# Optimization experiments

Measured on AMD Instinct MI355X. Metric: run time of the kernel, lower is better.

Reference implementation:

```python
import jax, jax.numpy as jnp
import numpy as np

V, L_MAX, D_MODEL, N_LAYER, N_STATE, EXPAND = 49408, 512, 768, 4, 16, 2
D_INNER = EXPAND * D_MODEL            # 1536
DT_RANK = -(-D_MODEL // 16)           # 48 ('auto' = ceil(d_model/16))
D_CONV = 4
B, T = 4, 256
EPS = 1e-5


def setup_inputs() -> dict:
    key = jax.random.key(0)
    ks = jax.random.split(key, 10)
    s = 0.02
    inp = {
        "input_ids": jax.random.randint(ks[0], (B, T), 0, V),
        "emb": jax.random.normal(ks[1], (V, D_MODEL), jnp.float32) * s,
        "pos_emb": jax.random.normal(ks[2], (1, L_MAX, D_MODEL), jnp.float32) * s,
        "in_proj_w": jax.random.normal(ks[3], (N_LAYER, 2 * D_INNER, D_MODEL), jnp.float32) * s,
        "conv_w": jax.random.normal(ks[4], (N_LAYER, D_INNER, D_CONV), jnp.float32) * s,
        "conv_b": jnp.zeros((N_LAYER, D_INNER), jnp.float32),
        "x_proj_w": jax.random.normal(ks[5], (N_LAYER, DT_RANK + 2 * N_STATE, D_INNER), jnp.float32) * s,
        "dt_proj_w": jax.random.normal(ks[6], (N_LAYER, D_INNER, DT_RANK), jnp.float32) * s,
        "dt_proj_b": jnp.full((N_LAYER, D_INNER), -4.6, jnp.float32),  # softplus(-4.6)~0.01, inside [dt_min,dt_max]
        # S4D-real init: A_log[l,d,n] = log(n+1)
        "A_log": jnp.tile(jnp.log(jnp.arange(1, N_STATE + 1, dtype=jnp.float32)), (N_LAYER, D_INNER, 1)),
        "D_skip": jnp.ones((N_LAYER, D_INNER), jnp.float32),
        "out_proj_w": jax.random.normal(ks[7], (N_LAYER, D_MODEL, D_INNER), jnp.float32) * s,
        "norm_w": jnp.ones((D_MODEL,), jnp.float32),
    }
    return inp


def _causal_dwconv(x, w, b):
    # x: (B, C, T), w: (C, K) depthwise, b: (C,) ; causal pad K-1 on the left
    out = jax.lax.conv_general_dilated(
        x, w[:, None, :], window_strides=(1,), padding=[(D_CONV - 1, 0)],
        feature_group_count=x.shape[1], dimension_numbers=("NCH", "OIH", "NCH"))
    return out + b[None, :, None]


def _selective_scan(deltaA, dBx, Cm):
    # deltaA, dBx: (B, T, D, N); Cm: (B, T, N) -> y: (B, T, D)
    def step(h, t_in):
        dA, dbx, c = t_in
        h = dA * h + dbx                          # (B, D, N)
        y = jnp.einsum("bdn,bn->bd", h, c)
        return h, y
    h0 = jnp.zeros(deltaA.shape[:1] + deltaA.shape[2:], deltaA.dtype)
    _, ys = jax.lax.scan(step, h0, (deltaA.swapaxes(0, 1), dBx.swapaxes(0, 1), Cm.swapaxes(0, 1)))
    return ys.swapaxes(0, 1)


def _mamba_block(x, ipw, cw, cb, xpw, dpw, dpb, A_log, Dp, opw):
    # x: (B, T, d_model)
    xz = jnp.einsum("btd,ed->bte", x, ipw)        # (B, T, 2*D_INNER)
    xi, z = jnp.split(xz, 2, axis=-1)
    xi = jax.nn.silu(_causal_dwconv(xi.swapaxes(1, 2), cw, cb)).swapaxes(1, 2)  # (B, T, D_INNER)
    x_dbl = jnp.einsum("btd,ed->bte", xi, xpw)    # (B, T, DT_RANK + 2N)
    dt, Bm, Cm = jnp.split(x_dbl, [DT_RANK, DT_RANK + N_STATE], axis=-1)
    dt = jax.nn.softplus(jnp.einsum("btr,dr->btd", dt, dpw) + dpb)              # (B, T, D_INNER)
    A = -jnp.exp(A_log)                            # (D_INNER, N)
    deltaA = jnp.exp(dt[..., None] * A)            # (B, T, D_INNER, N)
    dBx = dt[..., None] * Bm[:, :, None, :] * xi[..., None]                     # (B, T, D_INNER, N)
    y = _selective_scan(deltaA, dBx, Cm) + Dp * xi
    y = y * jax.nn.silu(z)
    return jnp.einsum("btd,ed->bte", y, opw)       # (B, T, d_model)


def reference(input_ids, emb, pos_emb, in_proj_w, conv_w, conv_b, x_proj_w,
              dt_proj_w, dt_proj_b, A_log, D_skip, out_proj_w, norm_w):
    Tlen = input_ids.shape[1]
    x = emb[input_ids] + pos_emb[:, :Tlen, :]
    for l in range(N_LAYER):
        x = x + _mamba_block(x, in_proj_w[l], conv_w[l], conv_b[l], x_proj_w[l],
                             dt_proj_w[l], dt_proj_b[l], A_log[l], D_skip[l], out_proj_w[l])
    # RMSNormGated with no gate -> plain RMSNorm
    x = x * jax.lax.rsqrt(jnp.mean(x * x, axis=-1, keepdims=True) + EPS) * norm_w
    return x
```

## Files before the change

### kernel.cpp

```cpp
#include <hip/hip_runtime.h>
#include <math.h>

#define TLEN 256
#define BATCH 4
#define DMODEL 768
#define DINNER 1536
#define NSTATE 16
#define DTRANK 48
#define NLAYER 4
#define NTOK 1024

#define S_IP 2359296
#define S_OP 1179648
#define S_XP2 196608
#define S_DT 98304
#define WL (S_IP + S_OP + S_XP2 + S_DT)

typedef __bf16 bf16x8 __attribute__((ext_vector_type(8)));
typedef float f32x4 __attribute__((ext_vector_type(4)));

__device__ inline unsigned short f2b(float f) {
    union { float f; unsigned u; } v;
    v.f = f;
    unsigned r = (v.u + 0x7fffu + ((v.u >> 16) & 1u)) >> 16;
    return (unsigned short)r;
}

__device__ inline void gload16(const void* g, void* l) {
    __builtin_amdgcn_global_load_lds(
        (const __attribute__((address_space(1))) void*)g,
        (__attribute__((address_space(3))) void*)l, 16, 0, 0);
}

__device__ inline float red16(float p) {
    p += __int_as_float(__builtin_amdgcn_update_dpp(0, __float_as_int(p), 0xB1, 0xf, 0xf, true));
    p += __int_as_float(__builtin_amdgcn_update_dpp(0, __float_as_int(p), 0x4E, 0xf, 0xf, true));
    p += __int_as_float(__builtin_amdgcn_update_dpp(0, __float_as_int(p), 0x124, 0xf, 0xf, true));
    p += __int_as_float(__builtin_amdgcn_update_dpp(0, __float_as_int(p), 0x128, 0xf, 0xf, true));
    return p;
}

__global__ __launch_bounds__(256) void embed_k(const int* __restrict__ ids,
                                               const float* __restrict__ emb,
                                               const float* __restrict__ pos,
                                               float* __restrict__ x,
                                               unsigned short* __restrict__ xb) {
    int idx = blockIdx.x * 256 + threadIdx.x;
    int d = idx % DMODEL;
    int bt = idx / DMODEL;
    int t = bt % TLEN;
    float v = emb[(size_t)ids[bt] * DMODEL + d] + pos[t * DMODEL + d];
    x[idx] = v;
    xb[idx] = f2b(v);
}

__global__ __launch_bounds__(256) void wconv_k(const float* __restrict__ ipw,
                                               const float* __restrict__ opw,
                                               const float* __restrict__ xpw,
                                               const float* __restrict__ dpw,
                                               unsigned short* __restrict__ w_all) {
    int l = blockIdx.y;
    int i4 = (blockIdx.x * 256 + threadIdx.x) * 4;
    unsigned short* wl = w_all + (size_t)l * WL;
    if (i4 < S_IP) {
        float4 v = *(const float4*)(ipw + (size_t)l * S_IP + i4);
        ushort4 o; o.x = f2b(v.x); o.y = f2b(v.y); o.z = f2b(v.z); o.w = f2b(v.w);
        *(ushort4*)(wl + i4) = o;
    } else if (i4 < S_IP + S_OP) {
        int i = i4 - S_IP;
        float4 v = *(const float4*)(opw + (size_t)l * S_OP + i);
        ushort4 o; o.x = f2b(v.x); o.y = f2b(v.y); o.z = f2b(v.z); o.w = f2b(v.w);
        *(ushort4*)(wl + S_IP + i) = o;
    } else if (i4 < S_IP + S_OP + S_XP2) {
        int i = i4 - S_IP - S_OP;
        int r = i / 1536, k = i % 1536;
        ushort4 o = {0, 0, 0, 0};
        if (r < 80) {
            float4 v = *(const float4*)(xpw + (size_t)l * (80 * 1536) + (size_t)r * 1536 + k);
            o.x = f2b(v.x); o.y = f2b(v.y); o.z = f2b(v.z); o.w = f2b(v.w);
        }
        *(ushort4*)(wl + S_IP + S_OP + i) = o;
    } else {
        int i = i4 - S_IP - S_OP - S_XP2;
        int r = i >> 6, k = i & 63;
        ushort4 o = {0, 0, 0, 0};
        if (k < DTRANK) {
            float4 v = *(const float4*)(dpw + (size_t)l * (DINNER * DTRANK) + (size_t)r * DTRANK + k);
            o.x = f2b(v.x); o.y = f2b(v.y); o.z = f2b(v.z); o.w = f2b(v.w);
        }
        *(ushort4*)(wl + S_IP + S_OP + S_XP2 + i) = o;
    }
}

template <int BM, int MODE>
__global__ __launch_bounds__(256) void mgemm_k(const unsigned short* __restrict__ A, int lda,
                                               const unsigned short* __restrict__ B, int ldb,
                                               int K,
                                               const float* __restrict__ bias,
                                               float* __restrict__ o0,
                                               unsigned short* __restrict__ o1) {
    constexpr int MI = BM / 32;
    __shared__ __align__(16) unsigned short Ab[2][BM * 64];
    __shared__ __align__(16) unsigned short Bb[2][64 * 64];
    __shared__ float Tt[(MODE == 1) ? 64 * 64 : 1];

    int tid = threadIdx.x;
    int lane = tid & 63;
    int wave = tid >> 6;
    int wm = (wave >> 1) * (BM / 2);
    int wn = (wave & 1) * 32;
    int bm = blockIdx.x * BM;
    int bn = blockIdx.y * 64;
    int fr = lane & 15;
    int fq = lane >> 4;
    int fk = fq * 8;
    int srow = lane >> 3;
    int scol = (lane & 7) * 8;

    f32x4 acc[MI][2] = {};

    auto stage = [&](int s, int k0) {
#pragma unroll
        for (int c = 0; c < BM / 32; ++c) {
            int r = wave * (BM / 4) + c * 8;
            gload16(A + (size_t)(bm + r + srow) * lda + k0 + scol, &Ab[s][r * 64]);
        }
#pragma unroll
        for (int c = 0; c < 2; ++c) {
            int r = wave * 16 + c * 8;
            gload16(B + (size_t)(bn + r + srow) * ldb + k0 + scol, &Bb[s][r * 64]);
        }
    };

    int nk = K >> 6;
    stage(0, 0);
    asm volatile("s_waitcnt vmcnt(0)" ::: "memory");
    __builtin_amdgcn_s_barrier();

    for (int t = 0; t < nk; ++t) {
        int cur = t & 1;
        if (t + 1 < nk) stage(cur ^ 1, (t + 1) * 64);
#pragma unroll
        for (int ks = 0; ks < 2; ++ks) {
            int kk = ks * 32 + fk;
            bf16x8 af[MI], bfr[2];
#pragma unroll
            for (int i = 0; i < MI; ++i)
                af[i] = *(const bf16x8*)&Ab[cur][(wm + i * 16 + fr) * 64 + kk];
#pragma unroll
            for (int j = 0; j < 2; ++j)
                bfr[j] = *(const bf16x8*)&Bb[cur][(wn + j * 16 + fr) * 64 + kk];
#pragma unroll
            for (int i = 0; i < MI; ++i)
#pragma unroll
                for (int j = 0; j < 2; ++j)
                    acc[i][j] = __builtin_amdgcn_mfma_f32_16x16x32_bf16(
                        af[i], bfr[j], acc[i][j], 0, 0, 0);
        }
        asm volatile("s_waitcnt vmcnt(0)" ::: "memory");
        __builtin_amdgcn_s_barrier();
    }

#pragma unroll
    for (int i = 0; i < MI; ++i) {
#pragma unroll
        for (int j = 0; j < 2; ++j) {
            int lc = wn + j * 16 + fr;
#pragma unroll
            for (int q = 0; q < 4; ++q) {
                int lr = wm + i * 16 + fq * 4 + q;
                float v = acc[i][j][q];
                if (MODE == 0) {
                    o0[(size_t)(bm + lr) * NTOK + bn + lc] = v;
                } else if (MODE == 1) {
                    int f = bm + lr;
                    if (f < 80) o0[(size_t)f * NTOK + bn + lc] = v;
                    Tt[lc * 64 + lr] = v;
                } else if (MODE == 2) {
                    float s = v + bias[bm + lr];
                    s = (s > 0.f) ? s + log1pf(__expf(-s)) : log1pf(__expf(s));
                    o0[(size_t)(bm + lr) * NTOK + bn + lc] = s;
                } else {
                    size_t idx = (size_t)(bm + lr) * DMODEL + bn + lc;
                    float nv = o0[idx] + v;
                    o0[idx] = nv;
                    o1[idx] = f2b(nv);
                }
            }
        }
    }
    if (MODE == 1) {
        __syncthreads();
        if (bm == 0) {
            int tok = tid >> 2;
            int fb = (tid & 3) * 16;
#pragma unroll
            for (int vv = 0; vv < 4; ++vv) {
                int f0 = fb + vv * 4;
                ushort4 o;
                o.x = f2b(Tt[tok * 64 + f0 + 0]);
                o.y = f2b(Tt[tok * 64 + f0 + 1]);
                o.z = f2b(Tt[tok * 64 + f0 + 2]);
                o.w = f2b(Tt[tok * 64 + f0 + 3]);
                *(ushort4*)(o1 + (size_t)(bn + tok) * 64 + f0) = o;
            }
        }
    }
}

__global__ __launch_bounds__(256) void conv_k(const float* __restrict__ xzT,
                                              const float* __restrict__ cw,
                                              const float* __restrict__ cb,
                                              unsigned short* __restrict__ xib) {
    __shared__ unsigned short tile[4][256];
    int tid = threadIdx.x;
    int ch = tid >> 6;
    int d = blockIdx.x * 4 + ch;
    int b = blockIdx.y;
    int t0 = (tid & 63) * 4;
    const float* src = xzT + (size_t)d * NTOK + b * TLEN + t0;
    float4 cur = *(const float4*)src;
    float4 prev = {0.f, 0.f, 0.f, 0.f};
    if (t0 > 0) prev = *(const float4*)(src - 4);
    float w0 = cw[d * 4 + 0], w1 = cw[d * 4 + 1], w2 = cw[d * 4 + 2], w3 = cw[d * 4 + 3];
    float bb = cb[d];
    float xw[8] = {prev.x, prev.y, prev.z, prev.w, cur.x, cur.y, cur.z, cur.w};
#pragma unroll
    for (int u = 0; u < 4; ++u) {
        float s = bb + w0 * xw[u + 1] + w1 * xw[u + 2] + w2 * xw[u + 3] + w3 * xw[u + 4];
        float v = s / (1.f + __expf(-s));
        tile[ch][t0 + u] = f2b(v);
    }
    __syncthreads();
    int t = tid;
    ushort4 o;
    o.x = tile[0][t]; o.y = tile[1][t]; o.z = tile[2][t]; o.w = tile[3][t];
    *(ushort4*)(xib + (size_t)(b * TLEN + t) * DINNER + blockIdx.x * 4) = o;
}

__global__ __launch_bounds__(512) void scan_k(const float* __restrict__ dtT,
                                              const float* __restrict__ xzT,
                                              const float* __restrict__ xdblT,
                                              const float* __restrict__ cw,
                                              const float* __restrict__ cb,
                                              const float* __restrict__ Alog,
                                              const float* __restrict__ Dsk,
                                              unsigned short* __restrict__ ybb) {
    __shared__ float yl[4][260];
    __shared__ float cum[4][260];
    __shared__ float hL[8][4][16];
    __shared__ float Pb[8][4][16];
    __shared__ float Hin[8][4][16];

    int tid = threadIdx.x;
    int c = tid >> 6;
    int lane = tid & 63;
    int ch = lane >> 4;
    int n = lane & 15;
    int d = blockIdx.x * 4 + ch;
    int b = blockIdx.y;
    int tl0 = c * 32;

    float a = -__expf(Alog[(size_t)d * NSTATE + n]);
    float Dv = Dsk[d];
    float w0 = cw[d * 4 + 0], w1 = cw[d * 4 + 1], w2 = cw[d * 4 + 2], w3 = cw[d * 4 + 3];
    float cbv = cb[d];
    const float* dtp = dtT + (size_t)d * NTOK + b * TLEN + tl0;
    const float* xzp = xzT + (size_t)d * NTOK + b * TLEN + tl0;
    const float* Bp = xdblT + (size_t)(DTRANK + n) * NTOK + b * TLEN + tl0;
    const float* Cp = xdblT + (size_t)(DTRANK + NSTATE + n) * NTOK + b * TLEN + tl0;

    float hm3 = 0.f, hm2 = 0.f, hm1 = 0.f;
    if (tl0 > 0) {
        float4 pv = *(const float4*)(xzp - 4);
        hm3 = pv.y; hm2 = pv.z; hm1 = pv.w;
    }

    float h = 0.f, cd = 0.f;
    for (int t8 = 0; t8 < 32; t8 += 8) {
        float4 d0 = *(const float4*)(dtp + t8), d1 = *(const float4*)(dtp + t8 + 4);
        float4 x0 = *(const float4*)(xzp + t8), x1 = *(const float4*)(xzp + t8 + 4);
        float4 B0 = *(const float4*)(Bp + t8), B1 = *(const float4*)(Bp + t8 + 4);
        float4 C0 = *(const float4*)(Cp + t8), C1 = *(const float4*)(Cp + t8 + 4);
        float dts[8] = {d0.x, d0.y, d0.z, d0.w, d1.x, d1.y, d1.z, d1.w};
        float xw[11] = {hm3, hm2, hm1, x0.x, x0.y, x0.z, x0.w, x1.x, x1.y, x1.z, x1.w};
        float Bs[8] = {B0.x, B0.y, B0.z, B0.w, B1.x, B1.y, B1.z, B1.w};
        float Cs[8] = {C0.x, C0.y, C0.z, C0.w, C1.x, C1.y, C1.z, C1.w};
#pragma unroll
        for (int u = 0; u < 8; ++u) {
            float s = cbv + w0 * xw[u] + w1 * xw[u + 1] + w2 * xw[u + 2] + w3 * xw[u + 3];
            float xi = s / (1.f + __expf(-s));
            float dtv = dts[u];
            cd += dtv;
            float dA = __expf(dtv * a);
            h = dA * h + (dtv * xi) * Bs[u];
            float p = red16(h * Cs[u]);
            if (n == 0) {
                yl[ch][tl0 + t8 + u] = p + Dv * xi;
                cum[ch][tl0 + t8 + u] = cd;
            }
        }
        hm3 = xw[8]; hm2 = xw[9]; hm1 = xw[10];
    }
    hL[c][ch][n] = h;
    Pb[c][ch][n] = __expf(a * cd);
    __syncthreads();
    if (c == 0) {
        float H = 0.f;
        Hin[0][ch][n] = 0.f;
#pragma unroll
        for (int cc = 1; cc < 8; ++cc) {
            H = Pb[cc - 1][ch][n] * H + hL[cc - 1][ch][n];
            Hin[cc][ch][n] = H;
        }
    }
    __syncthreads();
    float Hv = Hin[c][ch][n];
    const float* zp = xzT + (size_t)(DINNER + d) * NTOK + b * TLEN + tl0;
    for (int t8 = 0; t8 < 32; t8 += 8) {
        float4 C0 = *(const float4*)(Cp + t8), C1 = *(const float4*)(Cp + t8 + 4);
        float4 z0 = *(const float4*)(zp + t8), z1 = *(const float4*)(zp + t8 + 4);
        float Cs[8] = {C0.x, C0.y, C0.z, C0.w, C1.x, C1.y, C1.z, C1.w};
        float zs[8] = {z0.x, z0.y, z0.z, z0.w, z1.x, z1.y, z1.z, z1.w};
#pragma unroll
        for (int u = 0; u < 8; ++u) {
            float cdt = cum[ch][tl0 + t8 + u];
            float corr = red16(Cs[u] * __expf(a * cdt) * Hv);
            if (n == 0) {
                float y = yl[ch][tl0 + t8 + u] + corr;
                float zz = zs[u];
                y *= zz / (1.f + __expf(-zz));
                yl[ch][tl0 + t8 + u] = y;
            }
        }
    }
    __syncthreads();
    if (tid < 256) {
        int t = tid;
        ushort4 o;
        o.x = f2b(yl[0][t]);
        o.y = f2b(yl[1][t]);
        o.z = f2b(yl[2][t]);
        o.w = f2b(yl[3][t]);
        *(ushort4*)(ybb + (size_t)(b * TLEN + t) * DINNER + blockIdx.x * 4) = o;
    }
}

__global__ __launch_bounds__(256) void rmsnorm_k(const float* __restrict__ x,
                                                 const float* __restrict__ nw,
                                                 float* __restrict__ out) {
    int row = blockIdx.x;
    const float* xr = x + (size_t)row * DMODEL;
    int tid = threadIdx.x;
    float s = 0.f;
    for (int d = tid; d < DMODEL; d += 256) {
        float v = xr[d];
        s += v * v;
    }
#pragma unroll
    for (int off = 32; off >= 1; off >>= 1) s += __shfl_down(s, off);
    __shared__ float red[4];
    __shared__ float scale;
    int wid = tid >> 6, lane = tid & 63;
    if (lane == 0) red[wid] = s;
    __syncthreads();
    if (tid == 0) {
        float tot = red[0] + red[1] + red[2] + red[3];
        scale = rsqrtf(tot / (float)DMODEL + 1e-5f);
    }
    __syncthreads();
    float sc = scale;
    for (int d = tid; d < DMODEL; d += 256)
        out[(size_t)row * DMODEL + d] = xr[d] * sc * nw[d];
}

extern "C" void kernel_launch(void* const* d_in, const int* in_sizes, int n_in,
                              void* d_out, int out_size, void* d_ws, size_t ws_size,
                              hipStream_t stream) {
    const int* ids = (const int*)d_in[0];
    const float* emb = (const float*)d_in[1];
    const float* pos = (const float*)d_in[2];
    const float* ipw = (const float*)d_in[3];
    const float* cw = (const float*)d_in[4];
    const float* cb = (const float*)d_in[5];
    const float* xpw = (const float*)d_in[6];
    const float* dpw = (const float*)d_in[7];
    const float* dpb = (const float*)d_in[8];
    const float* Alog = (const float*)d_in[9];
    const float* Dsk = (const float*)d_in[10];
    const float* opw = (const float*)d_in[11];
    const float* nw = (const float*)d_in[12];

    float* x = (float*)d_ws;
    float* xzT = x + 786432;
    float* xdblT = xzT + 3145728;
    float* dtT = xdblT + 81920;
    unsigned short* xb = (unsigned short*)(dtT + 1572864);
    unsigned short* xib = xb + 786432;
    unsigned short* ybb = xib + 1572864;
    unsigned short* xdblb = ybb + 1572864;
    unsigned short* w_all = xdblb + 65536;

    wconv_k<<<dim3(WL / 1024, NLAYER), 256, 0, stream>>>(ipw, opw, xpw, dpw, w_all);
    embed_k<<<NTOK * DMODEL / 256, 256, 0, stream>>>(ids, emb, pos, x, xb);

    for (int l = 0; l < NLAYER; ++l) {
        const unsigned short* w_ip = w_all + (size_t)l * WL;
        const unsigned short* w_op = w_ip + S_IP;
        const unsigned short* w_xp = w_op + S_OP;
        const unsigned short* w_dt = w_xp + S_XP2;
        const float* cw_l = cw + (size_t)l * DINNER * 4;
        const float* cb_l = cb + (size_t)l * DINNER;
        const float* dpb_l = dpb + (size_t)l * DINNER;
        const float* Alog_l = Alog + (size_t)l * DINNER * NSTATE;
        const float* Dsk_l = Dsk + (size_t)l * DINNER;

        mgemm_k<64, 0><<<dim3(3072 / 64, NTOK / 64), 256, 0, stream>>>(
            w_ip, DMODEL, xb, DMODEL, DMODEL, nullptr, xzT, nullptr);
        conv_k<<<dim3(DINNER / 4, BATCH), 256, 0, stream>>>(xzT, cw_l, cb_l, xib);
        mgemm_k<64, 1><<<dim3(2, NTOK / 64), 256, 0, stream>>>(
            w_xp, DINNER, xib, DINNER, DINNER, nullptr, xdblT, xdblb);
        mgemm_k<64, 2><<<dim3(DINNER / 64, NTOK / 64), 256, 0, stream>>>(
            w_dt, 64, xdblb, 64, 64, dpb_l, dtT, nullptr);
        scan_k<<<dim3(DINNER / 4, BATCH), 512, 0, stream>>>(
            dtT, xzT, xdblT, cw_l, cb_l, Alog_l, Dsk_l, ybb);
        mgemm_k<64, 3><<<dim3(NTOK / 64, DMODEL / 64), 256, 0, stream>>>(
            ybb, DINNER, w_op, DINNER, DINNER, nullptr, x, xb);
    }

    rmsnorm_k<<<NTOK, 256, 0, stream>>>(x, nw, (float*)d_out);
}
```

Before: 527.2 us.

## Fuse conv into x_proj GEMM, fold dt_proj, store activations in bf16

Depthwise conv + SiLU is computed on the fly while staging the x_proj GEMM's B operand. The dt projection with softplus is then run inside the same kernel using the x_dbl tile kept in shared memory. The xz and dt intermediates are stored as bf16 instead of fp32 to halve their memory traffic, and the weight conversion and embedding kernels are merged into one launch. This removes separate conv and dt GEMM launches and their intermediate round trips. The cost is that the fused kernel runs only 16 blocks serially over all dt tiles, and bf16 storage loses some precision.

```diff
diff --git a/kernel.cpp b/kernel.cpp
--- a/kernel.cpp
+++ b/kernel.cpp
@@ -15,6 +15,9 @@
 #define S_XP2 196608
 #define S_DT 98304
 #define WL (S_IP + S_OP + S_XP2 + S_DT)
+#define NB_W (WL / 1024)
+#define NB_WALL (NB_W * NLAYER)
+#define NB_E (NTOK * DMODEL / 256)
 
 typedef __bf16 bf16x8 __attribute__((ext_vector_type(8)));
 typedef float f32x4 __attribute__((ext_vector_type(4)));
@@ -24,6 +27,11 @@
     v.f = f;
     unsigned r = (v.u + 0x7fffu + ((v.u >> 16) & 1u)) >> 16;
     return (unsigned short)r;
+}
+__device__ inline float b2f(unsigned short u) {
+    union { unsigned u; float f; } v;
+    v.u = ((unsigned)u) << 16;
+    return v.f;
 }
 
 __device__ inline void gload16(const void* g, void* l) {
@@ -40,27 +48,30 @@
     return p;
 }
 
-__global__ __launch_bounds__(256) void embed_k(const int* __restrict__ ids,
-                                               const float* __restrict__ emb,
-                                               const float* __restrict__ pos,
-                                               float* __restrict__ x,
-                                               unsigned short* __restrict__ xb) {
-    int idx = blockIdx.x * 256 + threadIdx.x;
-    int d = idx % DMODEL;
-    int bt = idx / DMODEL;
-    int t = bt % TLEN;
-    float v = emb[(size_t)ids[bt] * DMODEL + d] + pos[t * DMODEL + d];
-    x[idx] = v;
-    xb[idx] = f2b(v);
-}
-
-__global__ __launch_bounds__(256) void wconv_k(const float* __restrict__ ipw,
-                                               const float* __restrict__ opw,
-                                               const float* __restrict__ xpw,
-                                               const float* __restrict__ dpw,
-                                               unsigned short* __restrict__ w_all) {
-    int l = blockIdx.y;
-    int i4 = (blockIdx.x * 256 + threadIdx.x) * 4;
+__global__ __launch_bounds__(256) void prep_k(const float* __restrict__ ipw,
+                                              const float* __restrict__ opw,
+                                              const float* __restrict__ xpw,
+                                              const float* __restrict__ dpw,
+                                              const int* __restrict__ ids,
+                                              const float* __restrict__ emb,
+                                              const float* __restrict__ pos,
+                                              unsigned short* __restrict__ w_all,
+                                              float* __restrict__ x,
+                                              unsigned short* __restrict__ xb) {
+    int bid = blockIdx.x;
+    int tid = threadIdx.x;
+    if (bid >= NB_WALL) {
+        int idx = (bid - NB_WALL) * 256 + tid;
+        int d = idx % DMODEL;
+        int bt = idx / DMODEL;
+        int t = bt % TLEN;
+        float v = emb[(size_t)ids[bt] * DMODEL + d] + pos[t * DMODEL + d];
+        x[idx] = v;
+        xb[idx] = f2b(v);
+        return;
+    }
+    int l = bid / NB_W;
+    int i4 = ((bid % NB_W) * 256 + tid) * 4;
     unsigned short* wl = w_all + (size_t)l * WL;
     if (i4 < S_IP) {
         float4 v = *(const float4*)(ipw + (size_t)l * S_IP + i4);
@@ -92,24 +103,21 @@
     }
 }
 
-template <int BM, int MODE>
+template <int MODE>
 __global__ __launch_bounds__(256) void mgemm_k(const unsigned short* __restrict__ A, int lda,
                                                const unsigned short* __restrict__ B, int ldb,
                                                int K,
-                                               const float* __restrict__ bias,
                                                float* __restrict__ o0,
                                                unsigned short* __restrict__ o1) {
-    constexpr int MI = BM / 32;
-    __shared__ __align__(16) unsigned short Ab[2][BM * 64];
+    __shared__ __align__(16) unsigned short Ab[2][64 * 64];
     __shared__ __align__(16) unsigned short Bb[2][64 * 64];
-    __shared__ float Tt[(MODE == 1) ? 64 * 64 : 1];
 
     int tid = threadIdx.x;
     int lane = tid & 63;
     int wave = tid >> 6;
-    int wm = (wave >> 1) * (BM / 2);
+    int wm = (wave >> 1) * 32;
     int wn = (wave & 1) * 32;
-    int bm = blockIdx.x * BM;
+    int bm = blockIdx.x * 64;
     int bn = blockIdx.y * 64;
     int fr = lane & 15;
     int fq = lane >> 4;
@@ -117,17 +125,13 @@
     int srow = lane >> 3;
     int scol = (lane & 7) * 8;
 
-    f32x4 acc[MI][2] = {};
+    f32x4 acc[2][2] = {};
 
     auto stage = [&](int s, int k0) {
-#pragma unroll
-        for (int c = 0; c < BM / 32; ++c) {
-            int r = wave * (BM / 4) + c * 8;
-            gload16(A + (size_t)(bm + r + srow) * lda + k0 + scol, &Ab[s][r * 64]);
-        }
 #pragma unroll
         for (int c = 0; c < 2; ++c) {
             int r = wave * 16 + c * 8;
+            gload16(A + (size_t)(bm + r + srow) * lda + k0 + scol, &Ab[s][r * 64]);
             gload16(B + (size_t)(bn + r + srow) * ldb + k0 + scol, &Bb[s][r * 64]);
         }
     };
@@ -143,15 +147,15 @@
 #pragma unroll
         for (int ks = 0; ks < 2; ++ks) {
             int kk = ks * 32 + fk;
-            bf16x8 af[MI], bfr[2];
-#pragma unroll
-            for (int i = 0; i < MI; ++i)
+            bf16x8 af[2], bfr[2];
+#pragma unroll
+            for (int i = 0; i < 2; ++i)
                 af[i] = *(const bf16x8*)&Ab[cur][(wm + i * 16 + fr) * 64 + kk];
 #pragma unroll
             for (int j = 0; j < 2; ++j)
                 bfr[j] = *(const bf16x8*)&Bb[cur][(wn + j * 16 + fr) * 64 + kk];
 #pragma unroll
-            for (int i = 0; i < MI; ++i)
+            for (int i = 0; i < 2; ++i)
 #pragma unroll
                 for (int j = 0; j < 2; ++j)
                     acc[i][j] = __builtin_amdgcn_mfma_f32_16x16x32_bf16(
@@ -162,7 +166,7 @@
     }
 
 #pragma unroll
-    for (int i = 0; i < MI; ++i) {
+    for (int i = 0; i < 2; ++i) {
 #pragma unroll
         for (int j = 0; j < 2; ++j) {
             int lc = wn + j * 16 + fr;
@@ -171,15 +175,7 @@
                 int lr = wm + i * 16 + fq * 4 + q;
                 float v = acc[i][j][q];
                 if (MODE == 0) {
-                    o0[(size_t)(bm + lr) * NTOK + bn + lc] = v;
-                } else if (MODE == 1) {
-                    int f = bm + lr;
-                    if (f < 80) o0[(size_t)f * NTOK + bn + lc] = v;
-                    Tt[lc * 64 + lr] = v;
-                } else if (MODE == 2) {
-                    float s = v + bias[bm + lr];
-                    s = (s > 0.f) ? s + log1pf(__expf(-s)) : log1pf(__expf(s));
-                    o0[(size_t)(bm + lr) * NTOK + bn + lc] = s;
+                    o1[(size_t)(bm + lr) * NTOK + bn + lc] = f2b(v);
                 } else {
                     size_t idx = (size_t)(bm + lr) * DMODEL + bn + lc;
                     float nv = o0[idx] + v;
@@ -189,57 +185,179 @@
             }
         }
     }
-    if (MODE == 1) {
+}
+
+__global__ __launch_bounds__(256) void xproj_k(const unsigned short* __restrict__ xzT,
+                                               const unsigned short* __restrict__ w_xp,
+                                               const unsigned short* __restrict__ w_dt,
+                                               const float* __restrict__ dpb,
+                                               const float* __restrict__ cw,
+                                               const float* __restrict__ cb,
+                                               float* __restrict__ xdblT,
+                                               unsigned short* __restrict__ dtT) {
+    __shared__ __align__(16) unsigned short Ab[2][128 * 64];
+    __shared__ __align__(16) unsigned short Bb[2][64 * 64];
+    __shared__ __align__(16) unsigned short Tt[64 * 64];
+    __shared__ float dpb_s[DINNER];
+
+    int tid = threadIdx.x;
+    int lane = tid & 63;
+    int wave = tid >> 6;
+    int bn = blockIdx.x;
+    int tok0 = bn * 64;
+    int wm = (wave >> 1) * 64;
+    int wn = (wave & 1) * 32;
+    int fr = lane & 15;
+    int fq = lane >> 4;
+    int fk = fq * 8;
+    int srow = lane >> 3;
+    int scol = (lane & 7) * 8;
+
+    int cd_ = tid & 63;
+    int cg = tid >> 6;
+    bool atStart = ((bn & 3) == 0) && (cg == 0);
+
+    ushort4 bl[5];
+    float4 cw4;
+    float cbv;
+
+    auto stageA = [&](int s, int k0) {
+#pragma unroll
+        for (int c = 0; c < 4; ++c) {
+            int r = wave * 32 + c * 8;
+            gload16(w_xp + (size_t)(r + srow) * DINNER + k0 + scol, &Ab[s][r * 64]);
+        }
+    };
+    auto loadB = [&](int k0) {
+        int d = k0 + cd_;
+        const unsigned short* row = xzT + (size_t)d * NTOK + tok0 + cg * 16;
+        ushort4 z4 = {0, 0, 0, 0};
+        bl[0] = atStart ? z4 : *(const ushort4*)(row - 4);
+#pragma unroll
+        for (int c = 0; c < 4; ++c) bl[c + 1] = *(const ushort4*)(row + c * 4);
+        cw4 = *(const float4*)(cw + d * 4);
+        cbv = cb[d];
+    };
+    auto writeB = [&](int s) {
+        float xw[20];
+#pragma unroll
+        for (int c = 0; c < 5; ++c) {
+            xw[c * 4 + 0] = b2f(bl[c].x); xw[c * 4 + 1] = b2f(bl[c].y);
+            xw[c * 4 + 2] = b2f(bl[c].z); xw[c * 4 + 3] = b2f(bl[c].w);
+        }
+#pragma unroll
+        for (int u = 0; u < 16; ++u) {
+            float sv = cbv + cw4.x * xw[u + 1] + cw4.y * xw[u + 2] +
+                       cw4.z * xw[u + 3] + cw4.w * xw[u + 4];
+            float v = sv / (1.f + __expf(-sv));
+            Bb[s][(cg * 16 + u) * 64 + cd_] = f2b(v);
+        }
+    };
+
+    f32x4 acc[4][2] = {};
+    const int nk = DINNER / 64;
+
+    loadB(0);
+    stageA(0, 0);
+    writeB(0);
+    __syncthreads();
+
+    for (int t = 0; t < nk; ++t) {
+        int cur = t & 1;
+        if (t + 1 < nk) {
+            loadB((t + 1) * 64);
+            stageA(cur ^ 1, (t + 1) * 64);
+        }
+#pragma unroll
+        for (int ks = 0; ks < 2; ++ks) {
+            int kk = ks * 32 + fk;
+            bf16x8 af[4], bfr[2];
+#pragma unroll
+            for (int i = 0; i < 4; ++i)
+                af[i] = *(const bf16x8*)&Ab[cur][(wm + i * 16 + fr) * 64 + kk];
+#pragma unroll
+            for (int j = 0; j < 2; ++j)
+                bfr[j] = *(const bf16x8*)&Bb[cur][(wn + j * 16 + fr) * 64 + kk];
+#pragma unroll
+            for (int i = 0; i < 4; ++i)
+#pragma unroll
+                for (int j = 0; j < 2; ++j)
+                    acc[i][j] = __builtin_amdgcn_mfma_f32_16x16x32_bf16(
+                        af[i], bfr[j], acc[i][j], 0, 0, 0);
+        }
+        if (t + 1 < nk) writeB(cur ^ 1);
         __syncthreads();
-        if (bm == 0) {
-            int tok = tid >> 2;
-            int fb = (tid & 3) * 16;
-#pragma unroll
-            for (int vv = 0; vv < 4; ++vv) {
-                int f0 = fb + vv * 4;
-                ushort4 o;
-                o.x = f2b(Tt[tok * 64 + f0 + 0]);
-                o.y = f2b(Tt[tok * 64 + f0 + 1]);
-                o.z = f2b(Tt[tok * 64 + f0 + 2]);
-                o.w = f2b(Tt[tok * 64 + f0 + 3]);
-                *(ushort4*)(o1 + (size_t)(bn + tok) * 64 + f0) = o;
+    }
+
+#pragma unroll
+    for (int i = 0; i < 4; ++i) {
+#pragma unroll
+        for (int j = 0; j < 2; ++j) {
+            int lc = wn + j * 16 + fr;
+#pragma unroll
+            for (int q = 0; q < 4; ++q) {
+                int lr = wm + i * 16 + fq * 4 + q;
+                float v = acc[i][j][q];
+                if (lr < 64) Tt[lc * 64 + lr] = f2b(v);
+                if (lr >= 48 && lr < 80) xdblT[(size_t)lr * NTOK + tok0 + lc] = v;
             }
         }
     }
-}
-
-__global__ __launch_bounds__(256) void conv_k(const float* __restrict__ xzT,
-                                              const float* __restrict__ cw,
-                                              const float* __restrict__ cb,
-                                              unsigned short* __restrict__ xib) {
-    __shared__ unsigned short tile[4][256];
-    int tid = threadIdx.x;
-    int ch = tid >> 6;
-    int d = blockIdx.x * 4 + ch;
-    int b = blockIdx.y;
-    int t0 = (tid & 63) * 4;
-    const float* src = xzT + (size_t)d * NTOK + b * TLEN + t0;
-    float4 cur = *(const float4*)src;
-    float4 prev = {0.f, 0.f, 0.f, 0.f};
-    if (t0 > 0) prev = *(const float4*)(src - 4);
-    float w0 = cw[d * 4 + 0], w1 = cw[d * 4 + 1], w2 = cw[d * 4 + 2], w3 = cw[d * 4 + 3];
-    float bb = cb[d];
-    float xw[8] = {prev.x, prev.y, prev.z, prev.w, cur.x, cur.y, cur.z, cur.w};
-#pragma unroll
-    for (int u = 0; u < 4; ++u) {
-        float s = bb + w0 * xw[u + 1] + w1 * xw[u + 2] + w2 * xw[u + 3] + w3 * xw[u + 4];
-        float v = s / (1.f + __expf(-s));
-        tile[ch][t0 + u] = f2b(v);
-    }
-    __syncthreads();
-    int t = tid;
-    ushort4 o;
-    o.x = tile[0][t]; o.y = tile[1][t]; o.z = tile[2][t]; o.w = tile[3][t];
-    *(ushort4*)(xib + (size_t)(b * TLEN + t) * DINNER + blockIdx.x * 4) = o;
-}
-
-__global__ __launch_bounds__(512) void scan_k(const float* __restrict__ dtT,
-                                              const float* __restrict__ xzT,
+    for (int r = tid; r < DINNER; r += 256) dpb_s[r] = dpb[r];
+    __syncthreads();
+
+    int wm2 = (wave >> 1) * 32;
+    int wn2 = (wave & 1) * 32;
+    auto stageDt = [&](int s, int tile) {
+#pragma unroll
+        for (int c = 0; c < 2; ++c) {
+            int r = wave * 16 + c * 8;
+            gload16(w_dt + (size_t)(tile * 64 + r + srow) * 64 + scol, &Ab[s][r * 64]);
+        }
+    };
+    stageDt(0, 0);
+    __syncthreads();
+    for (int tile = 0; tile < 24; ++tile) {
+        int cur = tile & 1;
+        if (tile + 1 < 24) stageDt(cur ^ 1, tile + 1);
+        f32x4 a2[2][2] = {};
+#pragma unroll
+        for (int ks = 0; ks < 2; ++ks) {
+            int kk = ks * 32 + fk;
+            bf16x8 af[2], bfr[2];
+#pragma unroll
+            for (int i = 0; i < 2; ++i)
+                af[i] = *(const bf16x8*)&Ab[cur][(wm2 + i * 16 + fr) * 64 + kk];
+#pragma unroll
+            for (int j = 0; j < 2; ++j)
+                bfr[j] = *(const bf16x8*)&Tt[(wn2 + j * 16 + fr) * 64 + kk];
+#pragma unroll
+            for (int i = 0; i < 2; ++i)
+#pragma unroll
+                for (int j = 0; j < 2; ++j)
+                    a2[i][j] = __builtin_amdgcn_mfma_f32_16x16x32_bf16(
+                        af[i], bfr[j], a2[i][j], 0, 0, 0);
+        }
+#pragma unroll
+        for (int i = 0; i < 2; ++i) {
+#pragma unroll
+            for (int j = 0; j < 2; ++j) {
+                int tok = tok0 + wn2 + j * 16 + fr;
+#pragma unroll
+                for (int q = 0; q < 4; ++q) {
+                    int d = tile * 64 + wm2 + i * 16 + fq * 4 + q;
+                    float v = a2[i][j][q] + dpb_s[d];
+                    v = (v > 0.f) ? v + log1pf(__expf(-v)) : log1pf(__expf(v));
+                    dtT[(size_t)d * NTOK + tok] = f2b(v);
+                }
+            }
+        }
+        __syncthreads();
+    }
+}
+
+__global__ __launch_bounds__(512) void scan_k(const unsigned short* __restrict__ dtT,
+                                              const unsigned short* __restrict__ xzT,
                                               const float* __restrict__ xdblT,
                                               const float* __restrict__ cw,
                                               const float* __restrict__ cb,
@@ -265,31 +383,34 @@
     float Dv = Dsk[d];
     float w0 = cw[d * 4 + 0], w1 = cw[d * 4 + 1], w2 = cw[d * 4 + 2], w3 = cw[d * 4 + 3];
     float cbv = cb[d];
-    const float* dtp = dtT + (size_t)d * NTOK + b * TLEN + tl0;
-    const float* xzp = xzT + (size_t)d * NTOK + b * TLEN + tl0;
+    const unsigned short* dtp = dtT + (size_t)d * NTOK + b * TLEN + tl0;
+    const unsigned short* xzp = xzT + (size_t)d * NTOK + b * TLEN + tl0;
     const float* Bp = xdblT + (size_t)(DTRANK + n) * NTOK + b * TLEN + tl0;
     const float* Cp = xdblT + (size_t)(DTRANK + NSTATE + n) * NTOK + b * TLEN + tl0;
 
     float hm3 = 0.f, hm2 = 0.f, hm1 = 0.f;
     if (tl0 > 0) {
-        float4 pv = *(const float4*)(xzp - 4);
-        hm3 = pv.y; hm2 = pv.z; hm1 = pv.w;
+        ushort4 pv = *(const ushort4*)(xzp - 4);
+        hm3 = b2f(pv.y); hm2 = b2f(pv.z); hm1 = b2f(pv.w);
     }
 
     float h = 0.f, cd = 0.f;
     for (int t8 = 0; t8 < 32; t8 += 8) {
-        float4 d0 = *(const float4*)(dtp + t8), d1 = *(const float4*)(dtp + t8 + 4);
-        float4 x0 = *(const float4*)(xzp + t8), x1 = *(const float4*)(xzp + t8 + 4);
+        ushort4 dv0 = *(const ushort4*)(dtp + t8), dv1 = *(const ushort4*)(dtp + t8 + 4);
+        ushort4 xv0 = *(const ushort4*)(xzp + t8), xv1 = *(const ushort4*)(xzp + t8 + 4);
         float4 B0 = *(const float4*)(Bp + t8), B1 = *(const float4*)(Bp + t8 + 4);
         float4 C0 = *(const float4*)(Cp + t8), C1 = *(const float4*)(Cp + t8 + 4);
-        float dts[8] = {d0.x, d0.y, d0.z, d0.w, d1.x, d1.y, d1.z, d1.w};
-        float xw[11] = {hm3, hm2, hm1, x0.x, x0.y, x0.z, x0.w, x1.x, x1.y, x1.z, x1.w};
+        float dts[8] = {b2f(dv0.x), b2f(dv0.y), b2f(dv0.z), b2f(dv0.w),
+                        b2f(dv1.x), b2f(dv1.y), b2f(dv1.z), b2f(dv1.w)};
+        float xw[11] = {hm3, hm2, hm1,
+                        b2f(xv0.x), b2f(xv0.y), b2f(xv0.z), b2f(xv0.w),
+                        b2f(xv1.x), b2f(xv1.y), b2f(xv1.z), b2f(xv1.w)};
         float Bs[8] = {B0.x, B0.y, B0.z, B0.w, B1.x, B1.y, B1.z, B1.w};
         float Cs[8] = {C0.x, C0.y, C0.z, C0.w, C1.x, C1.y, C1.z, C1.w};
 #pragma unroll
         for (int u = 0; u < 8; ++u) {
-            float s = cbv + w0 * xw[u] + w1 * xw[u + 1] + w2 * xw[u + 2] + w3 * xw[u + 3];
-            float xi = s / (1.f + __expf(-s));
+            float sv = cbv + w0 * xw[u] + w1 * xw[u + 1] + w2 * xw[u + 2] + w3 * xw[u + 3];
+            float xi = sv / (1.f + __expf(-sv));
             float dtv = dts[u];
             cd += dtv;
             float dA = __expf(dtv * a);
@@ -316,12 +437,13 @@
     }
     __syncthreads();
     float Hv = Hin[c][ch][n];
-    const float* zp = xzT + (size_t)(DINNER + d) * NTOK + b * TLEN + tl0;
+    const unsigned short* zp = xzT + (size_t)(DINNER + d) * NTOK + b * TLEN + tl0;
     for (int t8 = 0; t8 < 32; t8 += 8) {
         float4 C0 = *(const float4*)(Cp + t8), C1 = *(const float4*)(Cp + t8 + 4);
-        float4 z0 = *(const float4*)(zp + t8), z1 = *(const float4*)(zp + t8 + 4);
+        ushort4 zv0 = *(const ushort4*)(zp + t8), zv1 = *(const ushort4*)(zp + t8 + 4);
         float Cs[8] = {C0.x, C0.y, C0.z, C0.w, C1.x, C1.y, C1.z, C1.w};
-        float zs[8] = {z0.x, z0.y, z0.z, z0.w, z1.x, z1.y, z1.z, z1.w};
+        float zs[8] = {b2f(zv0.x), b2f(zv0.y), b2f(zv0.z), b2f(zv0.w),
+                       b2f(zv1.x), b2f(zv1.y), b2f(zv1.z), b2f(zv1.w)};
 #pragma unroll
         for (int u = 0; u < 8; ++u) {
             float cdt = cum[ch][tl0 + t8 + u];
@@ -392,17 +514,15 @@
     const float* nw = (const float*)d_in[12];
 
     float* x = (float*)d_ws;
-    float* xzT = x + 786432;
-    float* xdblT = xzT + 3145728;
-    float* dtT = xdblT + 81920;
-    unsigned short* xb = (unsigned short*)(dtT + 1572864);
-    unsigned short* xib = xb + 786432;
-    unsigned short* ybb = xib + 1572864;
-    unsigned short* xdblb = ybb + 1572864;
-    unsigned short* w_all = xdblb + 65536;
-
-    wconv_k<<<dim3(WL / 1024, NLAYER), 256, 0, stream>>>(ipw, opw, xpw, dpw, w_all);
-    embed_k<<<NTOK * DMODEL / 256, 256, 0, stream>>>(ids, emb, pos, x, xb);
+    float* xdblT = x + 786432;
+    unsigned short* xb = (unsigned short*)(xdblT + 81920);
+    unsigned short* xzT = xb + 786432;
+    unsigned short* dtT = xzT + 3145728;
+    unsigned short* ybb = dtT + 1572864;
+    unsigned short* w_all = ybb + 1572864;
+
+    prep_k<<<NB_WALL + NB_E, 256, 0, stream>>>(ipw, opw, xpw, dpw, ids, emb, pos,
+                                               w_all, x, xb);
 
     for (int l = 0; l < NLAYER; ++l) {
         const unsigned short* w_ip = w_all + (size_t)l * WL;
@@ -415,17 +535,13 @@
         const float* Alog_l = Alog + (size_t)l * DINNER * NSTATE;
         const float* Dsk_l = Dsk + (size_t)l * DINNER;
 
-        mgemm_k<64, 0><<<dim3(3072 / 64, NTOK / 64), 256, 0, stream>>>(
-            w_ip, DMODEL, xb, DMODEL, DMODEL, nullptr, xzT, nullptr);
-        conv_k<<<dim3(DINNER / 4, BATCH), 256, 0, stream>>>(xzT, cw_l, cb_l, xib);
-        mgemm_k<64, 1><<<dim3(2, NTOK / 64), 256, 0, stream>>>(
-            w_xp, DINNER, xib, DINNER, DINNER, nullptr, xdblT, xdblb);
-        mgemm_k<64, 2><<<dim3(DINNER / 64, NTOK / 64), 256, 0, stream>>>(
-            w_dt, 64, xdblb, 64, 64, dpb_l, dtT, nullptr);
+        mgemm_k<0><<<dim3(3072 / 64, NTOK / 64), 256, 0, stream>>>(
+            w_ip, DMODEL, xb, DMODEL, DMODEL, nullptr, xzT);
+        xproj_k<<<16, 256, 0, stream>>>(xzT, w_xp, w_dt, dpb_l, cw_l, cb_l, xdblT, dtT);
         scan_k<<<dim3(DINNER / 4, BATCH), 512, 0, stream>>>(
             dtT, xzT, xdblT, cw_l, cb_l, Alog_l, Dsk_l, ybb);
-        mgemm_k<64, 3><<<dim3(NTOK / 64, DMODEL / 64), 256, 0, stream>>>(
-            ybb, DINNER, w_op, DINNER, DINNER, nullptr, x, xb);
+        mgemm_k<3><<<dim3(NTOK / 64, DMODEL / 64), 256, 0, stream>>>(
+            ybb, DINNER, w_op, DINNER, DINNER, x, xb);
     }
 
     rmsnorm_k<<<NTOK, 256, 0, stream>>>(x, nw, (float*)d_out);
```

Result: slower. 1.071 ms (+103.1%).

## Store xz and dt intermediates in bf16 and merge prep kernels

Applied to the files above, without the earlier changes.

The in_proj GEMM output (xz) and the softplus dt output are now written as bf16 instead of fp32. conv_k and scan_k read them as ushort4 and widen to float. This halves the traffic of the largest per-layer intermediates. The weight-conversion and embedding kernels are merged into one launch, and the MODE 1 GEMM skips writing unused dt-rank rows to fp32. The cost is bf16 rounding of the pre-activation x, the gate z and dt, which the scan's exponentials and cumulative sums may amplify.

```diff
diff --git a/kernel.cpp b/kernel.cpp
--- a/kernel.cpp
+++ b/kernel.cpp
@@ -15,6 +15,9 @@
 #define S_XP2 196608
 #define S_DT 98304
 #define WL (S_IP + S_OP + S_XP2 + S_DT)
+#define NB_W (WL / 1024)
+#define NB_WALL (NB_W * NLAYER)
+#define NB_E (NTOK * DMODEL / 256)
 
 typedef __bf16 bf16x8 __attribute__((ext_vector_type(8)));
 typedef float f32x4 __attribute__((ext_vector_type(4)));
@@ -24,6 +27,11 @@
     v.f = f;
     unsigned r = (v.u + 0x7fffu + ((v.u >> 16) & 1u)) >> 16;
     return (unsigned short)r;
+}
+__device__ inline float b2f(unsigned short u) {
+    union { unsigned u; float f; } v;
+    v.u = ((unsigned)u) << 16;
+    return v.f;
 }
 
 __device__ inline void gload16(const void* g, void* l) {
@@ -40,27 +48,30 @@
     return p;
 }
 
-__global__ __launch_bounds__(256) void embed_k(const int* __restrict__ ids,
-                                               const float* __restrict__ emb,
-                                               const float* __restrict__ pos,
-                                               float* __restrict__ x,
-                                               unsigned short* __restrict__ xb) {
-    int idx = blockIdx.x * 256 + threadIdx.x;
-    int d = idx % DMODEL;
-    int bt = idx / DMODEL;
-    int t = bt % TLEN;
-    float v = emb[(size_t)ids[bt] * DMODEL + d] + pos[t * DMODEL + d];
-    x[idx] = v;
-    xb[idx] = f2b(v);
-}
-
-__global__ __launch_bounds__(256) void wconv_k(const float* __restrict__ ipw,
-                                               const float* __restrict__ opw,
-                                               const float* __restrict__ xpw,
-                                               const float* __restrict__ dpw,
-                                               unsigned short* __restrict__ w_all) {
-    int l = blockIdx.y;
-    int i4 = (blockIdx.x * 256 + threadIdx.x) * 4;
+__global__ __launch_bounds__(256) void prep_k(const float* __restrict__ ipw,
+                                              const float* __restrict__ opw,
+                                              const float* __restrict__ xpw,
+                                              const float* __restrict__ dpw,
+                                              const int* __restrict__ ids,
+                                              const float* __restrict__ emb,
+                                              const float* __restrict__ pos,
+                                              unsigned short* __restrict__ w_all,
+                                              float* __restrict__ x,
+                                              unsigned short* __restrict__ xb) {
+    int bid = blockIdx.x;
+    int tid = threadIdx.x;
+    if (bid >= NB_WALL) {
+        int idx = (bid - NB_WALL) * 256 + tid;
+        int d = idx % DMODEL;
+        int bt = idx / DMODEL;
+        int t = bt % TLEN;
+        float v = emb[(size_t)ids[bt] * DMODEL + d] + pos[t * DMODEL + d];
+        x[idx] = v;
+        xb[idx] = f2b(v);
+        return;
+    }
+    int l = bid / NB_W;
+    int i4 = ((bid % NB_W) * 256 + tid) * 4;
     unsigned short* wl = w_all + (size_t)l * WL;
     if (i4 < S_IP) {
         float4 v = *(const float4*)(ipw + (size_t)l * S_IP + i4);
@@ -92,24 +103,23 @@
     }
 }
 
-template <int BM, int MODE>
+template <int MODE>
 __global__ __launch_bounds__(256) void mgemm_k(const unsigned short* __restrict__ A, int lda,
                                                const unsigned short* __restrict__ B, int ldb,
                                                int K,
                                                const float* __restrict__ bias,
                                                float* __restrict__ o0,
                                                unsigned short* __restrict__ o1) {
-    constexpr int MI = BM / 32;
-    __shared__ __align__(16) unsigned short Ab[2][BM * 64];
+    __shared__ __align__(16) unsigned short Ab[2][64 * 64];
     __shared__ __align__(16) unsigned short Bb[2][64 * 64];
     __shared__ float Tt[(MODE == 1) ? 64 * 64 : 1];
 
     int tid = threadIdx.x;
     int lane = tid & 63;
     int wave = tid >> 6;
-    int wm = (wave >> 1) * (BM / 2);
+    int wm = (wave >> 1) * 32;
     int wn = (wave & 1) * 32;
-    int bm = blockIdx.x * BM;
+    int bm = blockIdx.x * 64;
     int bn = blockIdx.y * 64;
     int fr = lane & 15;
     int fq = lane >> 4;
@@ -117,17 +127,13 @@
     int srow = lane >> 3;
     int scol = (lane & 7) * 8;
 
-    f32x4 acc[MI][2] = {};
+    f32x4 acc[2][2] = {};
 
     auto stage = [&](int s, int k0) {
-#pragma unroll
-        for (int c = 0; c < BM / 32; ++c) {
-            int r = wave * (BM / 4) + c * 8;
-            gload16(A + (size_t)(bm + r + srow) * lda + k0 + scol, &Ab[s][r * 64]);
-        }
 #pragma unroll
         for (int c = 0; c < 2; ++c) {
             int r = wave * 16 + c * 8;
+            gload16(A + (size_t)(bm + r + srow) * lda + k0 + scol, &Ab[s][r * 64]);
             gload16(B + (size_t)(bn + r + srow) * ldb + k0 + scol, &Bb[s][r * 64]);
         }
     };
@@ -143,15 +149,15 @@
 #pragma unroll
         for (int ks = 0; ks < 2; ++ks) {
             int kk = ks * 32 + fk;
-            bf16x8 af[MI], bfr[2];
-#pragma unroll
-            for (int i = 0; i < MI; ++i)
+            bf16x8 af[2], bfr[2];
+#pragma unroll
+            for (int i = 0; i < 2; ++i)
                 af[i] = *(const bf16x8*)&Ab[cur][(wm + i * 16 + fr) * 64 + kk];
 #pragma unroll
             for (int j = 0; j < 2; ++j)
                 bfr[j] = *(const bf16x8*)&Bb[cur][(wn + j * 16 + fr) * 64 + kk];
 #pragma unroll
-            for (int i = 0; i < MI; ++i)
+            for (int i = 0; i < 2; ++i)
 #pragma unroll
                 for (int j = 0; j < 2; ++j)
                     acc[i][j] = __builtin_amdgcn_mfma_f32_16x16x32_bf16(
@@ -162,7 +168,7 @@
     }
 
 #pragma unroll
-    for (int i = 0; i < MI; ++i) {
+    for (int i = 0; i < 2; ++i) {
 #pragma unroll
         for (int j = 0; j < 2; ++j) {
             int lc = wn + j * 16 + fr;
@@ -171,15 +177,15 @@
                 int lr = wm + i * 16 + fq * 4 + q;
                 float v = acc[i][j][q];
                 if (MODE == 0) {
-                    o0[(size_t)(bm + lr) * NTOK + bn + lc] = v;
+                    o1[(size_t)(bm + lr) * NTOK + bn + lc] = f2b(v);
                 } else if (MODE == 1) {
                     int f = bm + lr;
-                    if (f < 80) o0[(size_t)f * NTOK + bn + lc] = v;
+                    if (f >= DTRANK && f < 80) o0[(size_t)f * NTOK + bn + lc] = v;
                     Tt[lc * 64 + lr] = v;
                 } else if (MODE == 2) {
                     float s = v + bias[bm + lr];
                     s = (s > 0.f) ? s + log1pf(__expf(-s)) : log1pf(__expf(s));
-                    o0[(size_t)(bm + lr) * NTOK + bn + lc] = s;
+                    o1[(size_t)(bm + lr) * NTOK + bn + lc] = f2b(s);
                 } else {
                     size_t idx = (size_t)(bm + lr) * DMODEL + bn + lc;
                     float nv = o0[idx] + v;
@@ -208,7 +214,7 @@
     }
 }
 
-__global__ __launch_bounds__(256) void conv_k(const float* __restrict__ xzT,
+__global__ __launch_bounds__(256) void conv_k(const unsigned short* __restrict__ xzT,
                                               const float* __restrict__ cw,
                                               const float* __restrict__ cb,
                                               unsigned short* __restrict__ xib) {
@@ -218,13 +224,14 @@
     int d = blockIdx.x * 4 + ch;
     int b = blockIdx.y;
     int t0 = (tid & 63) * 4;
-    const float* src = xzT + (size_t)d * NTOK + b * TLEN + t0;
-    float4 cur = *(const float4*)src;
-    float4 prev = {0.f, 0.f, 0.f, 0.f};
-    if (t0 > 0) prev = *(const float4*)(src - 4);
+    const unsigned short* src = xzT + (size_t)d * NTOK + b * TLEN + t0;
+    ushort4 cur = *(const ushort4*)src;
+    ushort4 prev = {0, 0, 0, 0};
+    if (t0 > 0) prev = *(const ushort4*)(src - 4);
     float w0 = cw[d * 4 + 0], w1 = cw[d * 4 + 1], w2 = cw[d * 4 + 2], w3 = cw[d * 4 + 3];
     float bb = cb[d];
-    float xw[8] = {prev.x, prev.y, prev.z, prev.w, cur.x, cur.y, cur.z, cur.w};
+    float xw[8] = {b2f(prev.x), b2f(prev.y), b2f(prev.z), b2f(prev.w),
+                   b2f(cur.x), b2f(cur.y), b2f(cur.z), b2f(cur.w)};
 #pragma unroll
     for (int u = 0; u < 4; ++u) {
         float s = bb + w0 * xw[u + 1] + w1 * xw[u + 2] + w2 * xw[u + 3] + w3 * xw[u + 4];
@@ -238,8 +245,8 @@
     *(ushort4*)(xib + (size_t)(b * TLEN + t) * DINNER + blockIdx.x * 4) = o;
 }
 
-__global__ __launch_bounds__(512) void scan_k(const float* __restrict__ dtT,
-                                              const float* __restrict__ xzT,
+__global__ __launch_bounds__(512) void scan_k(const unsigned short* __restrict__ dtT,
+                                              const unsigned short* __restrict__ xzT,
                                               const float* __restrict__ xdblT,
                                               const float* __restrict__ cw,
                                               const float* __restrict__ cb,
@@ -265,31 +272,34 @@
     float Dv = Dsk[d];
     float w0 = cw[d * 4 + 0], w1 = cw[d * 4 + 1], w2 = cw[d * 4 + 2], w3 = cw[d * 4 + 3];
     float cbv = cb[d];
-    const float* dtp = dtT + (size_t)d * NTOK + b * TLEN + tl0;
-    const float* xzp = xzT + (size_t)d * NTOK + b * TLEN + tl0;
+    const unsigned short* dtp = dtT + (size_t)d * NTOK + b * TLEN + tl0;
+    const unsigned short* xzp = xzT + (size_t)d * NTOK + b * TLEN + tl0;
     const float* Bp = xdblT + (size_t)(DTRANK + n) * NTOK + b * TLEN + tl0;
     const float* Cp = xdblT + (size_t)(DTRANK + NSTATE + n) * NTOK + b * TLEN + tl0;
 
     float hm3 = 0.f, hm2 = 0.f, hm1 = 0.f;
     if (tl0 > 0) {
-        float4 pv = *(const float4*)(xzp - 4);
-        hm3 = pv.y; hm2 = pv.z; hm1 = pv.w;
+        ushort4 pv = *(const ushort4*)(xzp - 4);
+        hm3 = b2f(pv.y); hm2 = b2f(pv.z); hm1 = b2f(pv.w);
     }
 
     float h = 0.f, cd = 0.f;
     for (int t8 = 0; t8 < 32; t8 += 8) {
-        float4 d0 = *(const float4*)(dtp + t8), d1 = *(const float4*)(dtp + t8 + 4);
-        float4 x0 = *(const float4*)(xzp + t8), x1 = *(const float4*)(xzp + t8 + 4);
+        ushort4 dv0 = *(const ushort4*)(dtp + t8), dv1 = *(const ushort4*)(dtp + t8 + 4);
+        ushort4 xv0 = *(const ushort4*)(xzp + t8), xv1 = *(const ushort4*)(xzp + t8 + 4);
         float4 B0 = *(const float4*)(Bp + t8), B1 = *(const float4*)(Bp + t8 + 4);
         float4 C0 = *(const float4*)(Cp + t8), C1 = *(const float4*)(Cp + t8 + 4);
-        float dts[8] = {d0.x, d0.y, d0.z, d0.w, d1.x, d1.y, d1.z, d1.w};
-        float xw[11] = {hm3, hm2, hm1, x0.x, x0.y, x0.z, x0.w, x1.x, x1.y, x1.z, x1.w};
+        float dts[8] = {b2f(dv0.x), b2f(dv0.y), b2f(dv0.z), b2f(dv0.w),
+                        b2f(dv1.x), b2f(dv1.y), b2f(dv1.z), b2f(dv1.w)};
+        float xw[11] = {hm3, hm2, hm1,
+                        b2f(xv0.x), b2f(xv0.y), b2f(xv0.z), b2f(xv0.w),
+                        b2f(xv1.x), b2f(xv1.y), b2f(xv1.z), b2f(xv1.w)};
         float Bs[8] = {B0.x, B0.y, B0.z, B0.w, B1.x, B1.y, B1.z, B1.w};
         float Cs[8] = {C0.x, C0.y, C0.z, C0.w, C1.x, C1.y, C1.z, C1.w};
 #pragma unroll
         for (int u = 0; u < 8; ++u) {
-            float s = cbv + w0 * xw[u] + w1 * xw[u + 1] + w2 * xw[u + 2] + w3 * xw[u + 3];
-            float xi = s / (1.f + __expf(-s));
+            float sv = cbv + w0 * xw[u] + w1 * xw[u + 1] + w2 * xw[u + 2] + w3 * xw[u + 3];
+            float xi = sv / (1.f + __expf(-sv));
             float dtv = dts[u];
             cd += dtv;
             float dA = __expf(dtv * a);
@@ -316,12 +326,13 @@
     }
     __syncthreads();
     float Hv = Hin[c][ch][n];
-    const float* zp = xzT + (size_t)(DINNER + d) * NTOK + b * TLEN + tl0;
+    const unsigned short* zp = xzT + (size_t)(DINNER + d) * NTOK + b * TLEN + tl0;
     for (int t8 = 0; t8 < 32; t8 += 8) {
         float4 C0 = *(const float4*)(Cp + t8), C1 = *(const float4*)(Cp + t8 + 4);
-        float4 z0 = *(const float4*)(zp + t8), z1 = *(const float4*)(zp + t8 + 4);
+        ushort4 zv0 = *(const ushort4*)(zp + t8), zv1 = *(const ushort4*)(zp + t8 + 4);
         float Cs[8] = {C0.x, C0.y, C0.z, C0.w, C1.x, C1.y, C1.z, C1.w};
-        float zs[8] = {z0.x, z0.y, z0.z, z0.w, z1.x, z1.y, z1.z, z1.w};
+        float zs[8] = {b2f(zv0.x), b2f(zv0.y), b2f(zv0.z), b2f(zv0.w),
+                       b2f(zv1.x), b2f(zv1.y), b2f(zv1.z), b2f(zv1.w)};
 #pragma unroll
         for (int u = 0; u < 8; ++u) {
             float cdt = cum[ch][tl0 + t8 + u];
@@ -392,17 +403,17 @@
     const float* nw = (const float*)d_in[12];
 
     float* x = (float*)d_ws;
-    float* xzT = x + 786432;
-    float* xdblT = xzT + 3145728;
-    float* dtT = xdblT + 81920;
-    unsigned short* xb = (unsigned short*)(dtT + 1572864);
-    unsigned short* xib = xb + 786432;
-    unsigned short* ybb = xib + 1572864;
+    float* xdblT = x + 786432;
+    unsigned short* xb = (unsigned short*)(xdblT + 81920);
+    unsigned short* xzT = xb + 786432;
+    unsigned short* xib = xzT + 3145728;
+    unsigned short* dtT = xib + 1572864;
+    unsigned short* ybb = dtT + 1572864;
     unsigned short* xdblb = ybb + 1572864;
     unsigned short* w_all = xdblb + 65536;
 
-    wconv_k<<<dim3(WL / 1024, NLAYER), 256, 0, stream>>>(ipw, opw, xpw, dpw, w_all);
-    embed_k<<<NTOK * DMODEL / 256, 256, 0, stream>>>(ids, emb, pos, x, xb);
+    prep_k<<<NB_WALL + NB_E, 256, 0, stream>>>(ipw, opw, xpw, dpw, ids, emb, pos,
+                                               w_all, x, xb);
 
     for (int l = 0; l < NLAYER; ++l) {
         const unsigned short* w_ip = w_all + (size_t)l * WL;
@@ -415,16 +426,16 @@
         const float* Alog_l = Alog + (size_t)l * DINNER * NSTATE;
         const float* Dsk_l = Dsk + (size_t)l * DINNER;
 
-        mgemm_k<64, 0><<<dim3(3072 / 64, NTOK / 64), 256, 0, stream>>>(
-            w_ip, DMODEL, xb, DMODEL, DMODEL, nullptr, xzT, nullptr);
+        mgemm_k<0><<<dim3(3072 / 64, NTOK / 64), 256, 0, stream>>>(
+            w_ip, DMODEL, xb, DMODEL, DMODEL, nullptr, nullptr, xzT);
         conv_k<<<dim3(DINNER / 4, BATCH), 256, 0, stream>>>(xzT, cw_l, cb_l, xib);
-        mgemm_k<64, 1><<<dim3(2, NTOK / 64), 256, 0, stream>>>(
+        mgemm_k<1><<<dim3(2, NTOK / 64), 256, 0, stream>>>(
             w_xp, DINNER, xib, DINNER, DINNER, nullptr, xdblT, xdblb);
-        mgemm_k<64, 2><<<dim3(DINNER / 64, NTOK / 64), 256, 0, stream>>>(
-            w_dt, 64, xdblb, 64, 64, dpb_l, dtT, nullptr);
+        mgemm_k<2><<<dim3(DINNER / 64, NTOK / 64), 256, 0, stream>>>(
+            w_dt, 64, xdblb, 64, 64, dpb_l, nullptr, dtT);
         scan_k<<<dim3(DINNER / 4, BATCH), 512, 0, stream>>>(
             dtT, xzT, xdblT, cw_l, cb_l, Alog_l, Dsk_l, ybb);
-        mgemm_k<64, 3><<<dim3(NTOK / 64, DMODEL / 64), 256, 0, stream>>>(
+        mgemm_k<3><<<dim3(NTOK / 64, DMODEL / 64), 256, 0, stream>>>(
             ybb, DINNER, w_op, DINNER, DINNER, nullptr, x, xb);
     }
 
```

Measured after the change: 514.8 us. -2.4%, faster.
